# Performance work log

Hardware: AMD Instinct MI355X
Metric: run time of the kernel (lower is better)

Reference implementation:

```python
import jax, jax.numpy as jnp
import numpy as np


def setup_inputs() -> dict:
    key = jax.random.key(0)
    k1, k2 = jax.random.split(key)
    decoder_hidden = jax.random.normal(k1, (16, 1024, 1024), dtype=jnp.float32)
    encoder_outputs = jax.random.normal(k2, (16, 2048, 1024), dtype=jnp.float32)
    return {"decoder_hidden": decoder_hidden, "encoder_outputs": encoder_outputs}


def reference(decoder_hidden, encoder_outputs):
    # scores: [B, Q, K] = decoder_hidden @ encoder_outputs^T (no scaling, per source)
    scores = jnp.einsum('bqd,bkd->bqk', decoder_hidden, encoder_outputs)
    attn = jax.nn.softmax(scores, axis=-1)
    # context: [B, Q, D]
    context = jnp.einsum('bqk,bkd->bqd', attn, encoder_outputs)
    return (context, attn)
```

## Files before the change

### kernel.cpp

```cpp
#include <hip/hip_runtime.h>


typedef __attribute__((ext_vector_type(8))) short s8v;
typedef __attribute__((ext_vector_type(4))) float f32x4;
typedef __attribute__((ext_vector_type(8))) unsigned short us8;
typedef __attribute__((ext_vector_type(4))) unsigned short us4;

__device__ inline unsigned short f2bf(float f) {
    unsigned u = __builtin_bit_cast(unsigned, f);
    u += 0x7FFFu + ((u >> 16) & 1u);
    return (unsigned short)(u >> 16);
}
__device__ inline float bf2f(unsigned short h) {
    return __builtin_bit_cast(float, (unsigned)h << 16);
}

__device__ __forceinline__ s8v lds_read128(unsigned addr) {
    s8v d;
    asm volatile("ds_read_b128 %0, %1" : "=v"(d) : "v"(addr));
    return d;
}

__global__ __launch_bounds__(256)
void split_convert(const float* __restrict__ x, unsigned short* __restrict__ hi,
                   unsigned short* __restrict__ lo, int n4)
{
    int i = blockIdx.x * 256 + threadIdx.x;
    const int stride = gridDim.x * 256;
    for (; i < n4; i += stride) {
        const float4 v = reinterpret_cast<const float4*>(x)[i];
        us4 h, l;
        h.x = f2bf(v.x); l.x = f2bf(v.x - bf2f(h.x));
        h.y = f2bf(v.y); l.y = f2bf(v.y - bf2f(h.y));
        h.z = f2bf(v.z); l.z = f2bf(v.z - bf2f(h.z));
        h.w = f2bf(v.w); l.w = f2bf(v.w - bf2f(h.w));
        reinterpret_cast<us4*>(hi)[i] = h;
        reinterpret_cast<us4*>(lo)[i] = l;
    }
}

__global__ __launch_bounds__(256)
void split_convert_enc(const float* __restrict__ enc,
                       unsigned short* __restrict__ encH,
                       unsigned short* __restrict__ encL,
                       unsigned short* __restrict__ encT)
{
    __shared__ unsigned short S[64][72];
    const int b  = blockIdx.z;
    const int kt = blockIdx.x;
    const int dt = blockIdx.y;
    const int tid = threadIdx.x;

    const int r   = tid >> 2;
    const int c16 = (tid & 3) * 16;

    const size_t inoff = (size_t)b * 2048 * 1024 + (size_t)(kt * 64 + r) * 1024 + dt * 64 + c16;
    const float4* src = reinterpret_cast<const float4*>(enc + inoff);

    us8 h0, h1, l0, l1;
    #pragma unroll
    for (int q = 0; q < 2; ++q) {
        const float4 a = src[q * 2 + 0];
        const float4 c = src[q * 2 + 1];
        us8& h = q ? h1 : h0;
        us8& l = q ? l1 : l0;
        h[0] = f2bf(a.x); l[0] = f2bf(a.x - bf2f(h[0]));
        h[1] = f2bf(a.y); l[1] = f2bf(a.y - bf2f(h[1]));
        h[2] = f2bf(a.z); l[2] = f2bf(a.z - bf2f(h[2]));
        h[3] = f2bf(a.w); l[3] = f2bf(a.w - bf2f(h[3]));
        h[4] = f2bf(c.x); l[4] = f2bf(c.x - bf2f(h[4]));
        h[5] = f2bf(c.y); l[5] = f2bf(c.y - bf2f(h[5]));
        h[6] = f2bf(c.z); l[6] = f2bf(c.z - bf2f(h[6]));
        h[7] = f2bf(c.w); l[7] = f2bf(c.w - bf2f(h[7]));
    }
    *reinterpret_cast<us8*>(&encH[inoff])     = h0;
    *reinterpret_cast<us8*>(&encH[inoff + 8]) = h1;
    *reinterpret_cast<us8*>(&encL[inoff])     = l0;
    *reinterpret_cast<us8*>(&encL[inoff + 8]) = l1;
    *reinterpret_cast<us8*>(&S[r][c16])     = h0;
    *reinterpret_cast<us8*>(&S[r][c16 + 8]) = h1;
    __syncthreads();

    const int d   = tid >> 2;
    const int k16 = (tid & 3) * 16;
    us8 w0, w1;
    #pragma unroll
    for (int j = 0; j < 8; ++j) { w0[j] = S[k16 + j][d]; w1[j] = S[k16 + 8 + j][d]; }
    const size_t outoff = (size_t)b * 1024 * 2048 + (size_t)(dt * 64 + d) * 2048 + kt * 64 + k16;
    *reinterpret_cast<us8*>(&encT[outoff])     = w0;
    *reinterpret_cast<us8*>(&encT[outoff + 8]) = w1;
}

template<int NPASS, int KPP, int NXT, int NYT>
__global__ __launch_bounds__(512, 2)
void gemm_nt_256(const unsigned short* __restrict__ A0,
                 const unsigned short* __restrict__ A1,
                 const unsigned short* __restrict__ A2,
                 const unsigned short* __restrict__ B0,
                 const unsigned short* __restrict__ B1,
                 const unsigned short* __restrict__ B2,
                 float* __restrict__ Out,
                 const int ldA, const int ldB, const int ldO,
                 const long long sA, const long long sB, const long long sO)
{
    constexpr int TPP = KPP / 32;
    constexpr int NT  = NPASS * TPP;
    extern __shared__ unsigned short smem[];

    int flat = blockIdx.x + NXT * (blockIdx.y + NYT * (int)blockIdx.z);
    const int nwg = NXT * NYT * (int)gridDim.z;
    flat = (flat & 7) * (nwg >> 3) + (flat >> 3);
    const int nt = flat % NXT;
    const int mt = (flat / NXT) % NYT;
    const int b  = flat / (NXT * NYT);

    const int tid = threadIdx.x, lane = tid & 63, wid = tid >> 6;
    const int wm = wid >> 2, wn = wid & 3;

    const size_t arow = (size_t)b * sA + (size_t)(mt * 256) * ldA;
    const size_t brow = (size_t)b * sB + (size_t)(nt * 256) * ldB;
    const unsigned short* Ap0 = A0 + arow;
    const unsigned short* Ap1 = A1 + arow;
    const unsigned short* Ap2 = A2 + arow;
    const unsigned short* Bp0 = B0 + brow;
    const unsigned short* Bp1 = B1 + brow;
    const unsigned short* Bp2 = B2 + brow;

    const int ci0 = tid, ci1 = 512 + tid;
    const int r0 = ci0 >> 2, r1 = ci1 >> 2;
    const int cs0 = ((ci0 & 3) ^ ((r0 >> 1) & 3)) * 8;
    const int cs1 = ((ci1 & 3) ^ ((r1 >> 1) & 3)) * 8;
    const int aoff0 = r0 * ldA + cs0, aoff1 = r1 * ldA + cs1;
    const int boff0 = r0 * ldB + cs0, boff1 = r1 * ldB + cs1;
    const int wd0 = wid * 512;
    const int wd1 = 4096 + wid * 512;

    auto stageA = [&](int t) {
        const int p  = t / TPP;
        const int k0 = (t % TPP) * 32;
        const unsigned short* As = (p == 0) ? Ap0 : (p == 1 ? Ap1 : Ap2);
        unsigned short* d = smem + (t & 3) * 16384;
        __builtin_amdgcn_global_load_lds(
            (const __attribute__((address_space(1))) void*)(As + k0 + aoff0),
            (__attribute__((address_space(3))) void*)(d + wd0), 16, 0, 0);
        __builtin_amdgcn_global_load_lds(
            (const __attribute__((address_space(1))) void*)(As + k0 + aoff1),
            (__attribute__((address_space(3))) void*)(d + wd1), 16, 0, 0);
    };
    auto stageB = [&](int t) {
        const int p  = t / TPP;
        const int k0 = (t % TPP) * 32;
        const unsigned short* Bs = (p == 0) ? Bp0 : (p == 1 ? Bp1 : Bp2);
        unsigned short* d = smem + (t & 3) * 16384 + 8192;
        __builtin_amdgcn_global_load_lds(
            (const __attribute__((address_space(1))) void*)(Bs + k0 + boff0),
            (__attribute__((address_space(3))) void*)(d + wd0), 16, 0, 0);
        __builtin_amdgcn_global_load_lds(
            (const __attribute__((address_space(1))) void*)(Bs + k0 + boff1),
            (__attribute__((address_space(3))) void*)(d + wd1), 16, 0, 0);
    };

    const int fr = lane & 15;
    const int kc = lane >> 4;
    unsigned offA[8], offB[4];
    #pragma unroll
    for (int m = 0; m < 8; ++m) {
        const int R = wm * 128 + m * 16 + fr;
        offA[m] = (unsigned)(R * 64) + ((unsigned)(kc ^ ((R >> 1) & 3)) << 4);
    }
    #pragma unroll
    for (int n = 0; n < 4; ++n) {
        const int R = wn * 64 + n * 16 + fr;
        offB[n] = 16384u + (unsigned)(R * 64) + ((unsigned)(kc ^ ((R >> 1) & 3)) << 4);
    }

    const unsigned lds0 =
        (unsigned)(uintptr_t)(__attribute__((address_space(3))) unsigned short*)smem;

    f32x4 acc[8][4];
    #pragma unroll
    for (int m = 0; m < 8; ++m)
        #pragma unroll
        for (int n = 0; n < 4; ++n) acc[m][n] = (f32x4){0.f, 0.f, 0.f, 0.f};

    stageA(0); stageB(0); stageA(1); stageB(1); stageA(2); stageB(2);
    asm volatile("s_waitcnt vmcnt(4)" ::: "memory");
    __builtin_amdgcn_s_barrier();

    s8v fA[8], fB[4], gA[8], gB[4];
    #pragma unroll
    for (int n = 0; n < 4; ++n) fB[n] = lds_read128(lds0 + offB[n]);
    #pragma unroll
    for (int m = 0; m < 8; ++m) fA[m] = lds_read128(lds0 + offA[m]);

    auto issue_reads = [&](const int t, s8v (&na)[8], s8v (&nb)[4]) {
        const unsigned nbase = lds0 + (unsigned)((t + 1) & 3) * 32768u;
        #pragma unroll
        for (int n = 0; n < 4; ++n) nb[n] = lds_read128(nbase + offB[n]);
        #pragma unroll
        for (int m = 0; m < 8; ++m) na[m] = lds_read128(nbase + offA[m]);
    };
    auto do_mfma = [&](s8v (&ca)[8], s8v (&cb)[4]) {
        __builtin_amdgcn_s_setprio(1);
        #pragma unroll
        for (int m = 0; m < 8; ++m)
            #pragma unroll
            for (int n = 0; n < 4; ++n)
                acc[m][n] = __builtin_amdgcn_mfma_f32_16x16x32_bf16(ca[m], cb[n], acc[m][n], 0, 0, 0);
        __builtin_amdgcn_s_setprio(0);
    };
    auto tail_sync = [&](const int t) {
        if (t + 3 < NT)      asm volatile("s_waitcnt vmcnt(4)" ::: "memory");
        else if (t + 2 < NT) asm volatile("s_waitcnt vmcnt(0)" ::: "memory");
        __builtin_amdgcn_s_barrier();
    };

    auto bodyA = [&](const int t, s8v (&ca)[8], s8v (&cb)[4],
                     s8v (&na)[8], s8v (&nb)[4], const bool reads) {
        if (t + 3 < NT) { stageA(t + 3); stageB(t + 3); }
        if (reads) {
            issue_reads(t, na, nb);
            asm volatile("s_waitcnt lgkmcnt(12)" ::: "memory");
        } else {
            asm volatile("s_waitcnt lgkmcnt(0)" ::: "memory");
        }
        __builtin_amdgcn_sched_barrier(0);
        do_mfma(ca, cb);
        __builtin_amdgcn_sched_barrier(0);
        tail_sync(t);
    };
    auto bodyB = [&](const int t, s8v (&ca)[8], s8v (&cb)[4],
                     s8v (&na)[8], s8v (&nb)[4], const bool reads) {
        if (t + 3 < NT) { stageA(t + 3); stageB(t + 3); }
        asm volatile("s_waitcnt lgkmcnt(0)" ::: "memory");
        __builtin_amdgcn_sched_barrier(0);
        do_mfma(ca, cb);
        __builtin_amdgcn_sched_barrier(0);
        if (reads) issue_reads(t, na, nb);
        tail_sync(t);
    };

    if (wid < 4) {
        for (int tt = 0; tt < NT; tt += 2) {
            bodyA(tt,     fA, fB, gA, gB, true);
            bodyA(tt + 1, gA, gB, fA, fB, tt + 2 < NT);
        }
    } else {
        for (int tt = 0; tt < NT; tt += 2) {
            bodyB(tt,     fA, fB, gA, gB, true);
            bodyB(tt + 1, gA, gB, fA, fB, tt + 2 < NT);
        }
    }

    float* Ob = Out + (size_t)b * sO + (size_t)(mt * 256 + wm * 128) * ldO + nt * 256 + wn * 64;
    const int cr = (lane >> 4) << 2;
    const int cc = lane & 15;
    #pragma unroll
    for (int m = 0; m < 8; ++m)
        #pragma unroll
        for (int n = 0; n < 4; ++n)
            #pragma unroll
            for (int r = 0; r < 4; ++r)
                Ob[(size_t)(m * 16 + cr + r) * ldO + n * 16 + cc] = acc[m][n][r];
}

__global__ __launch_bounds__(256)
void softmax_rows_bf(float* __restrict__ P, unsigned short* __restrict__ Pb)
{
    float* p = P + (size_t)blockIdx.x * 2048;
    unsigned short* pb = Pb + (size_t)blockIdx.x * 2048;
    const int tid = threadIdx.x;

    float4 v0 = *reinterpret_cast<const float4*>(&p[tid * 4]);
    float4 v1 = *reinterpret_cast<const float4*>(&p[1024 + tid * 4]);

    float m = fmaxf(fmaxf(fmaxf(v0.x, v0.y), fmaxf(v0.z, v0.w)),
                    fmaxf(fmaxf(v1.x, v1.y), fmaxf(v1.z, v1.w)));
    #pragma unroll
    for (int off = 32; off; off >>= 1) m = fmaxf(m, __shfl_xor(m, off));

    __shared__ float red[8];
    const int wid = tid >> 6;
    if ((tid & 63) == 0) red[wid] = m;
    __syncthreads();
    m = fmaxf(fmaxf(red[0], red[1]), fmaxf(red[2], red[3]));

    v0.x = __expf(v0.x - m); v0.y = __expf(v0.y - m);
    v0.z = __expf(v0.z - m); v0.w = __expf(v0.w - m);
    v1.x = __expf(v1.x - m); v1.y = __expf(v1.y - m);
    v1.z = __expf(v1.z - m); v1.w = __expf(v1.w - m);

    float s = ((v0.x + v0.y) + (v0.z + v0.w)) + ((v1.x + v1.y) + (v1.z + v1.w));
    #pragma unroll
    for (int off = 32; off; off >>= 1) s += __shfl_xor(s, off);
    if ((tid & 63) == 0) red[4 + wid] = s;
    __syncthreads();
    const float inv = 1.0f / ((red[4] + red[5]) + (red[6] + red[7]));

    v0.x *= inv; v0.y *= inv; v0.z *= inv; v0.w *= inv;
    v1.x *= inv; v1.y *= inv; v1.z *= inv; v1.w *= inv;
    *reinterpret_cast<float4*>(&p[tid * 4]) = v0;
    *reinterpret_cast<float4*>(&p[1024 + tid * 4]) = v1;

    us4 h0, h1;
    h0.x = f2bf(v0.x); h0.y = f2bf(v0.y); h0.z = f2bf(v0.z); h0.w = f2bf(v0.w);
    h1.x = f2bf(v1.x); h1.y = f2bf(v1.y); h1.z = f2bf(v1.z); h1.w = f2bf(v1.w);
    *reinterpret_cast<us4*>(&pb[tid * 4]) = h0;
    *reinterpret_cast<us4*>(&pb[1024 + tid * 4]) = h1;
}

#define BM 128
#define BN 128
#define BK 32
#define LDT 132

template <bool TRANSB>
__global__ __launch_bounds__(256, 2)
void gemm_tile(const float* __restrict__ X, const float* __restrict__ Y,
               float* __restrict__ Out,
               int ldX, int ldY, int ldO, int KD,
               long long strideX, long long strideY, long long strideO)
{
    __shared__ float As[BK][LDT];
    __shared__ float Bs[BK][LDT];
    const int b  = blockIdx.z;
    const int mt = blockIdx.y;
    const int nt = blockIdx.x;
    const float* Xb = X + (size_t)b * strideX + (size_t)mt * BM * ldX;
    const float* Yb = TRANSB ? (Y + (size_t)b * strideY + (size_t)nt * BN * ldY)
                             : (Y + (size_t)b * strideY + (size_t)nt * BN);
    float* Ob = Out + (size_t)b * strideO + (size_t)mt * BM * ldO + (size_t)nt * BN;
    const int tid = threadIdx.x;
    const int tx = tid & 15;
    const int ty = tid >> 4;
    const int sr = tid >> 3;
    const int sc = (tid & 7) << 2;
    const int br = tid >> 5;
    const int bc = (tid & 31) << 2;
    float acc[8][8];
    #pragma unroll
    for (int i = 0; i < 8; ++i)
        #pragma unroll
        for (int j = 0; j < 8; ++j) acc[i][j] = 0.f;
    for (int k0 = 0; k0 < KD; k0 += BK) {
        #pragma unroll
        for (int p = 0; p < 4; ++p) {
            const float4 v = *reinterpret_cast<const float4*>(
                &Xb[(size_t)(sr + 32 * p) * ldX + k0 + sc]);
            As[sc + 0][sr + 32 * p] = v.x;
            As[sc + 1][sr + 32 * p] = v.y;
            As[sc + 2][sr + 32 * p] = v.z;
            As[sc + 3][sr + 32 * p] = v.w;
        }
        if (TRANSB) {
            #pragma unroll
            for (int p = 0; p < 4; ++p) {
                const float4 v = *reinterpret_cast<const float4*>(
                    &Yb[(size_t)(sr + 32 * p) * ldY + k0 + sc]);
                Bs[sc + 0][sr + 32 * p] = v.x;
                Bs[sc + 1][sr + 32 * p] = v.y;
                Bs[sc + 2][sr + 32 * p] = v.z;
                Bs[sc + 3][sr + 32 * p] = v.w;
            }
        } else {
            #pragma unroll
            for (int p = 0; p < 4; ++p) {
                const float4 v = *reinterpret_cast<const float4*>(
                    &Yb[(size_t)(k0 + br + 8 * p) * ldY + bc]);
                *reinterpret_cast<float4*>(&Bs[br + 8 * p][bc]) = v;
            }
        }
        __syncthreads();
        #pragma unroll 8
        for (int kk = 0; kk < BK; ++kk) {
            const float4 a0 = *reinterpret_cast<const float4*>(&As[kk][ty * 4]);
            const float4 a1 = *reinterpret_cast<const float4*>(&As[kk][64 + ty * 4]);
            const float4 b0 = *reinterpret_cast<const float4*>(&Bs[kk][tx * 4]);
            const float4 b1 = *reinterpret_cast<const float4*>(&Bs[kk][64 + tx * 4]);
            const float av[8] = {a0.x, a0.y, a0.z, a0.w, a1.x, a1.y, a1.z, a1.w};
            const float bv[8] = {b0.x, b0.y, b0.z, b0.w, b1.x, b1.y, b1.z, b1.w};
            #pragma unroll
            for (int i = 0; i < 8; ++i)
                #pragma unroll
                for (int j = 0; j < 8; ++j)
                    acc[i][j] = fmaf(av[i], bv[j], acc[i][j]);
        }
        __syncthreads();
    }
    #pragma unroll
    for (int i = 0; i < 8; ++i) {
        const int r = (i < 4) ? (ty * 4 + i) : (64 + ty * 4 + (i - 4));
        const float4 w0 = make_float4(acc[i][0], acc[i][1], acc[i][2], acc[i][3]);
        const float4 w1 = make_float4(acc[i][4], acc[i][5], acc[i][6], acc[i][7]);
        *reinterpret_cast<float4*>(&Ob[(size_t)r * ldO + tx * 4])      = w0;
        *reinterpret_cast<float4*>(&Ob[(size_t)r * ldO + 64 + tx * 4]) = w1;
    }
}

__global__ __launch_bounds__(256)
void softmax_rows(float* __restrict__ P)
{
    float* p = P + (size_t)blockIdx.x * 2048;
    const int tid = threadIdx.x;
    float4 v0 = *reinterpret_cast<const float4*>(&p[tid * 4]);
    float4 v1 = *reinterpret_cast<const float4*>(&p[1024 + tid * 4]);
    float m = fmaxf(fmaxf(fmaxf(v0.x, v0.y), fmaxf(v0.z, v0.w)),
                    fmaxf(fmaxf(v1.x, v1.y), fmaxf(v1.z, v1.w)));
    #pragma unroll
    for (int off = 32; off; off >>= 1) m = fmaxf(m, __shfl_xor(m, off));
    __shared__ float red[8];
    const int wid = tid >> 6;
    if ((tid & 63) == 0) red[wid] = m;
    __syncthreads();
    m = fmaxf(fmaxf(red[0], red[1]), fmaxf(red[2], red[3]));
    v0.x = __expf(v0.x - m); v0.y = __expf(v0.y - m);
    v0.z = __expf(v0.z - m); v0.w = __expf(v0.w - m);
    v1.x = __expf(v1.x - m); v1.y = __expf(v1.y - m);
    v1.z = __expf(v1.z - m); v1.w = __expf(v1.w - m);
    float s = ((v0.x + v0.y) + (v0.z + v0.w)) + ((v1.x + v1.y) + (v1.z + v1.w));
    #pragma unroll
    for (int off = 32; off; off >>= 1) s += __shfl_xor(s, off);
    if ((tid & 63) == 0) red[4 + wid] = s;
    __syncthreads();
    const float inv = 1.0f / ((red[4] + red[5]) + (red[6] + red[7]));
    v0.x *= inv; v0.y *= inv; v0.z *= inv; v0.w *= inv;
    v1.x *= inv; v1.y *= inv; v1.z *= inv; v1.w *= inv;
    *reinterpret_cast<float4*>(&p[tid * 4]) = v0;
    *reinterpret_cast<float4*>(&p[1024 + tid * 4]) = v1;
}

extern "C" void kernel_launch(void* const* d_in, const int* in_sizes, int n_in,
                              void* d_out, int out_size, void* d_ws, size_t ws_size,
                              hipStream_t stream)
{
    const float* dec = (const float*)d_in[0];
    const float* enc = (const float*)d_in[1];
    float* ctx  = (float*)d_out;
    float* attn = ctx + (size_t)16 * 1024 * 1024;

    const long long DECN = 16LL * 1024 * 1024;
    const long long ENCN = 16LL * 2048 * 1024;
    const size_t NEED = (size_t)(2 * DECN + 4 * ENCN) * 2;

    if (ws_size >= NEED) {
        unsigned short* decH  = (unsigned short*)d_ws;
        unsigned short* decL  = decH + DECN;
        unsigned short* encH  = decL + DECN;
        unsigned short* encL  = encH + ENCN;
        unsigned short* encT  = encL + ENCN;
        unsigned short* attnB = encT + ENCN;

        hipFuncSetAttribute((const void*)&gemm_nt_256<3, 1024, 8, 4>,
                            hipFuncAttributeMaxDynamicSharedMemorySize, 131072);
        hipFuncSetAttribute((const void*)&gemm_nt_256<1, 2048, 4, 4>,
                            hipFuncAttributeMaxDynamicSharedMemorySize, 131072);

        split_convert<<<2048, 256, 0, stream>>>(dec, decH, decL, (int)(DECN / 4));
        split_convert_enc<<<dim3(32, 16, 16), 256, 0, stream>>>(enc, encH, encL, encT);

        gemm_nt_256<3, 1024, 8, 4><<<dim3(8, 4, 16), 512, 131072, stream>>>(
            decH, decH, decL, encH, encL, encH, attn,
            1024, 1024, 2048,
            1024LL * 1024, 2048LL * 1024, 1024LL * 2048);

        softmax_rows_bf<<<16 * 1024, 256, 0, stream>>>(attn, attnB);

        gemm_nt_256<1, 2048, 4, 4><<<dim3(4, 4, 16), 512, 131072, stream>>>(
            attnB, attnB, attnB, encT, encT, encT, ctx,
            2048, 2048, 1024,
            1024LL * 2048, 1024LL * 2048, 1024LL * 1024);
    } else {
        gemm_tile<true><<<dim3(2048 / BN, 1024 / BM, 16), 256, 0, stream>>>(
            dec, enc, attn, 1024, 1024, 2048, 1024,
            1024LL * 1024, 2048LL * 1024, 1024LL * 2048);
        softmax_rows<<<dim3(16 * 1024), 256, 0, stream>>>(attn);
        gemm_tile<false><<<dim3(1024 / BN, 1024 / BM, 16), 256, 0, stream>>>(
            attn, enc, ctx, 2048, 1024, 1024, 2048,
            1024LL * 2048, 2048LL * 1024, 1024LL * 1024);
    }
}
```

Before: 419.7 us.

## Restructure bf16 GEMM mainloop into 8-phase ping-pong schedule with 64-wide K tiles

Replaces the 4-stage, 32-wide-K GEMM pipeline (split into producer/consumer wave roles) with a double-buffered 64-wide-K tile. Each iteration is broken into eight phases in which all waves interleave quarter-tile LDS reads, global-to-LDS loads and MFMA bursts, with barriers between phases. The LDS swizzle changes to an 8-way XOR over 128-byte rows. The aim is to hide LDS and global latency behind MFMA work and cut barrier overhead per K step. The cost is many more barriers per iteration and only two buffers instead of four, so global loads have less time to arrive.

```diff
diff --git a/kernel.cpp b/kernel.cpp
--- a/kernel.cpp
+++ b/kernel.cpp
@@ -19,6 +19,52 @@
     s8v d;
     asm volatile("ds_read_b128 %0, %1" : "=v"(d) : "v"(addr));
     return d;
+}
+__device__ __forceinline__ void gld16(const unsigned short* src, unsigned short* dstLds) {
+    __builtin_amdgcn_global_load_lds(
+        (const __attribute__((address_space(1))) void*)src,
+        (__attribute__((address_space(3))) void*)dstLds, 16, 0, 0);
+}
+
+#define LGKM(n)  asm volatile("s_waitcnt lgkmcnt(" #n ")" ::: "memory")
+#define VMC(n)   asm volatile("s_waitcnt vmcnt(" #n ")" ::: "memory")
+#define SB0      __builtin_amdgcn_sched_barrier(0)
+#define BARR     __builtin_amdgcn_s_barrier()
+
+template<int MH, int NH>
+__device__ __forceinline__ void mfma16(f32x4 (&acc)[8][4], const s8v (&a)[8], const s8v (&b)[4])
+{
+    __builtin_amdgcn_s_setprio(1);
+    #pragma unroll
+    for (int kf = 0; kf < 2; ++kf)
+        #pragma unroll
+        for (int mp = 0; mp < 4; ++mp)
+            #pragma unroll
+            for (int np = 0; np < 2; ++np)
+                acc[MH * 4 + mp][NH * 2 + np] = __builtin_amdgcn_mfma_f32_16x16x32_bf16(
+                    a[mp * 2 + kf], b[np * 2 + kf], acc[MH * 4 + mp][NH * 2 + np], 0, 0, 0);
+    __builtin_amdgcn_s_setprio(0);
+}
+
+template<int D, int MH>
+__device__ __forceinline__ void readA(s8v (&a)[8], unsigned abase, unsigned cb0, unsigned cb1)
+{
+    const unsigned base = abase + D * 65536u + MH * 8192u;
+    #pragma unroll
+    for (int mp = 0; mp < 4; ++mp) {
+        a[mp * 2 + 0] = lds_read128(base + mp * 2048u + cb0);
+        a[mp * 2 + 1] = lds_read128(base + mp * 2048u + cb1);
+    }
+}
+template<int D, int NH>
+__device__ __forceinline__ void readB(s8v (&b)[4], unsigned bbase, unsigned cb0, unsigned cb1)
+{
+    const unsigned base = bbase + D * 65536u + NH * 4096u;
+    #pragma unroll
+    for (int np = 0; np < 2; ++np) {
+        b[np * 2 + 0] = lds_read128(base + np * 2048u + cb0);
+        b[np * 2 + 1] = lds_read128(base + np * 2048u + cb1);
+    }
 }
 
 __global__ __launch_bounds__(256)
@@ -91,20 +137,20 @@
     *reinterpret_cast<us8*>(&encT[outoff + 8]) = w1;
 }
 
-template<int NPASS, int KPP, int NXT, int NYT>
+template<int NPASS, int KSP, int NXT, int NYT>
 __global__ __launch_bounds__(512, 2)
-void gemm_nt_256(const unsigned short* __restrict__ A0,
-                 const unsigned short* __restrict__ A1,
-                 const unsigned short* __restrict__ A2,
-                 const unsigned short* __restrict__ B0,
-                 const unsigned short* __restrict__ B1,
-                 const unsigned short* __restrict__ B2,
+void gemm_nt_8ph(const unsigned short* __restrict__ A0p,
+                 const unsigned short* __restrict__ A1p,
+                 const unsigned short* __restrict__ A2p,
+                 const unsigned short* __restrict__ B0p,
+                 const unsigned short* __restrict__ B1p,
+                 const unsigned short* __restrict__ B2p,
                  float* __restrict__ Out,
                  const int ldA, const int ldB, const int ldO,
                  const long long sA, const long long sB, const long long sO)
 {
-    constexpr int TPP = KPP / 32;
-    constexpr int NT  = NPASS * TPP;
+    constexpr int NK    = NPASS * KSP;
+    constexpr int NITER = NK / 2;
     extern __shared__ unsigned short smem[];
 
     int flat = blockIdx.x + NXT * (blockIdx.y + NYT * (int)blockIdx.z);
@@ -116,66 +162,45 @@
 
     const int tid = threadIdx.x, lane = tid & 63, wid = tid >> 6;
     const int wm = wid >> 2, wn = wid & 3;
+    const int fr = lane & 15, kc = lane >> 4;
 
     const size_t arow = (size_t)b * sA + (size_t)(mt * 256) * ldA;
     const size_t brow = (size_t)b * sB + (size_t)(nt * 256) * ldB;
-    const unsigned short* Ap0 = A0 + arow;
-    const unsigned short* Ap1 = A1 + arow;
-    const unsigned short* Ap2 = A2 + arow;
-    const unsigned short* Bp0 = B0 + brow;
-    const unsigned short* Bp1 = B1 + brow;
-    const unsigned short* Bp2 = B2 + brow;
-
-    const int ci0 = tid, ci1 = 512 + tid;
-    const int r0 = ci0 >> 2, r1 = ci1 >> 2;
-    const int cs0 = ((ci0 & 3) ^ ((r0 >> 1) & 3)) * 8;
-    const int cs1 = ((ci1 & 3) ^ ((r1 >> 1) & 3)) * 8;
-    const int aoff0 = r0 * ldA + cs0, aoff1 = r1 * ldA + cs1;
-    const int boff0 = r0 * ldB + cs0, boff1 = r1 * ldB + cs1;
-    const int wd0 = wid * 512;
-    const int wd1 = 4096 + wid * 512;
-
-    auto stageA = [&](int t) {
-        const int p  = t / TPP;
-        const int k0 = (t % TPP) * 32;
-        const unsigned short* As = (p == 0) ? Ap0 : (p == 1 ? Ap1 : Ap2);
-        unsigned short* d = smem + (t & 3) * 16384;
-        __builtin_amdgcn_global_load_lds(
-            (const __attribute__((address_space(1))) void*)(As + k0 + aoff0),
-            (__attribute__((address_space(3))) void*)(d + wd0), 16, 0, 0);
-        __builtin_amdgcn_global_load_lds(
-            (const __attribute__((address_space(1))) void*)(As + k0 + aoff1),
-            (__attribute__((address_space(3))) void*)(d + wd1), 16, 0, 0);
+    const unsigned short* Ap0 = A0p + arow;
+    const unsigned short* Ap1 = A1p + arow;
+    const unsigned short* Ap2 = A2p + arow;
+    const unsigned short* Bp0 = B0p + brow;
+    const unsigned short* Bp1 = B1p + brow;
+    const unsigned short* Bp2 = B2p + brow;
+
+    const int srow = tid >> 3;
+    const int sc   = ((tid & 7) ^ (srow & 7)) * 8;
+    const int offA0 = srow * ldA + sc, offA1 = offA0 + 64 * ldA;
+    const int offB0 = srow * ldB + sc, offB1 = offB0 + 64 * ldB;
+
+    auto STAGEA = [&](int ks, int h) {
+        const int p = ks / KSP;
+        const unsigned short* s = ((p == 0) ? Ap0 : (p == 1) ? Ap1 : Ap2)
+                                  + (size_t)(h * 128) * ldA + (ks - p * KSP) * 64;
+        unsigned short* d = smem + ((ks & 1) * 32768 + h * 8192) + wid * 512;
+        gld16(s + offA0, d);
+        gld16(s + offA1, d + 4096);
     };
-    auto stageB = [&](int t) {
-        const int p  = t / TPP;
-        const int k0 = (t % TPP) * 32;
-        const unsigned short* Bs = (p == 0) ? Bp0 : (p == 1 ? Bp1 : Bp2);
-        unsigned short* d = smem + (t & 3) * 16384 + 8192;
-        __builtin_amdgcn_global_load_lds(
-            (const __attribute__((address_space(1))) void*)(Bs + k0 + boff0),
-            (__attribute__((address_space(3))) void*)(d + wd0), 16, 0, 0);
-        __builtin_amdgcn_global_load_lds(
-            (const __attribute__((address_space(1))) void*)(Bs + k0 + boff1),
-            (__attribute__((address_space(3))) void*)(d + wd1), 16, 0, 0);
+    auto STAGEB = [&](int ks, int h) {
+        const int p = ks / KSP;
+        const unsigned short* s = ((p == 0) ? Bp0 : (p == 1) ? Bp1 : Bp2)
+                                  + (size_t)(h * 128) * ldB + (ks - p * KSP) * 64;
+        unsigned short* d = smem + ((ks & 1) * 32768 + 16384 + h * 8192) + wid * 512;
+        gld16(s + offB0, d);
+        gld16(s + offB1, d + 4096);
     };
-
-    const int fr = lane & 15;
-    const int kc = lane >> 4;
-    unsigned offA[8], offB[4];
-    #pragma unroll
-    for (int m = 0; m < 8; ++m) {
-        const int R = wm * 128 + m * 16 + fr;
-        offA[m] = (unsigned)(R * 64) + ((unsigned)(kc ^ ((R >> 1) & 3)) << 4);
-    }
-    #pragma unroll
-    for (int n = 0; n < 4; ++n) {
-        const int R = wn * 64 + n * 16 + fr;
-        offB[n] = 16384u + (unsigned)(R * 64) + ((unsigned)(kc ^ ((R >> 1) & 3)) << 4);
-    }
 
     const unsigned lds0 =
         (unsigned)(uintptr_t)(__attribute__((address_space(3))) unsigned short*)smem;
+    const unsigned cb0 = (unsigned)((kc ^ (fr & 7)) * 16);
+    const unsigned cb1 = cb0 ^ 64u;
+    const unsigned abase = lds0 + wm * 16384u + fr * 128u;
+    const unsigned bbase = lds0 + 32768u + (wn >> 1) * 16384u + (wn & 1) * 8192u + fr * 128u;
 
     f32x4 acc[8][4];
     #pragma unroll
@@ -183,74 +208,61 @@
         #pragma unroll
         for (int n = 0; n < 4; ++n) acc[m][n] = (f32x4){0.f, 0.f, 0.f, 0.f};
 
-    stageA(0); stageB(0); stageA(1); stageB(1); stageA(2); stageB(2);
-    asm volatile("s_waitcnt vmcnt(4)" ::: "memory");
-    __builtin_amdgcn_s_barrier();
-
-    s8v fA[8], fB[4], gA[8], gB[4];
-    #pragma unroll
-    for (int n = 0; n < 4; ++n) fB[n] = lds_read128(lds0 + offB[n]);
-    #pragma unroll
-    for (int m = 0; m < 8; ++m) fA[m] = lds_read128(lds0 + offA[m]);
-
-    auto issue_reads = [&](const int t, s8v (&na)[8], s8v (&nb)[4]) {
-        const unsigned nbase = lds0 + (unsigned)((t + 1) & 3) * 32768u;
-        #pragma unroll
-        for (int n = 0; n < 4; ++n) nb[n] = lds_read128(nbase + offB[n]);
-        #pragma unroll
-        for (int m = 0; m < 8; ++m) na[m] = lds_read128(nbase + offA[m]);
+    s8v a[8], b0[4], b1[4];
+
+    STAGEA(0, 0); STAGEA(0, 1); STAGEB(0, 0); STAGEB(0, 1);
+    STAGEB(1, 0); STAGEB(1, 1); STAGEA(1, 0);
+    VMC(6);
+    BARR;
+
+    auto iter = [&](const int t, const bool last) {
+        const int ks0 = 2 * t;
+        readA<0, 0>(a, abase, cb0, cb1);
+        readB<0, 0>(b0, bbase, cb0, cb1);
+        STAGEA(ks0 + 1, 1);
+        LGKM(8); SB0; BARR; LGKM(0); SB0;
+        mfma16<0, 0>(acc, a, b0);
+        BARR;
+        readB<0, 1>(b1, bbase, cb0, cb1);
+        if (!last) STAGEB(ks0 + 2, 0);
+        SB0; BARR; LGKM(0); SB0;
+        mfma16<0, 1>(acc, a, b1);
+        BARR;
+        readA<0, 1>(a, abase, cb0, cb1);
+        if (!last) STAGEB(ks0 + 2, 1);
+        LGKM(4); SB0; BARR; LGKM(0); SB0;
+        mfma16<1, 0>(acc, a, b0);
+        BARR;
+        if (!last) STAGEA(ks0 + 2, 0);
+        if (last) { VMC(0); } else { VMC(6); }
+        SB0; BARR;
+        mfma16<1, 1>(acc, a, b1);
+        BARR;
+        readA<1, 0>(a, abase, cb0, cb1);
+        readB<1, 0>(b0, bbase, cb0, cb1);
+        if (!last) STAGEA(ks0 + 2, 1);
+        LGKM(8); SB0; BARR; LGKM(0); SB0;
+        mfma16<0, 0>(acc, a, b0);
+        BARR;
+        readB<1, 1>(b1, bbase, cb0, cb1);
+        if (!last) STAGEB(ks0 + 3, 0);
+        SB0; BARR; LGKM(0); SB0;
+        mfma16<0, 1>(acc, a, b1);
+        BARR;
+        readA<1, 1>(a, abase, cb0, cb1);
+        if (!last) STAGEB(ks0 + 3, 1);
+        LGKM(4); SB0; BARR; LGKM(0); SB0;
+        mfma16<1, 0>(acc, a, b0);
+        BARR;
+        if (!last) STAGEA(ks0 + 3, 0);
+        if (last) { VMC(0); } else { VMC(6); }
+        SB0; BARR;
+        mfma16<1, 1>(acc, a, b1);
+        BARR;
     };
-    auto do_mfma = [&](s8v (&ca)[8], s8v (&cb)[4]) {
-        __builtin_amdgcn_s_setprio(1);
-        #pragma unroll
-        for (int m = 0; m < 8; ++m)
-            #pragma unroll
-            for (int n = 0; n < 4; ++n)
-                acc[m][n] = __builtin_amdgcn_mfma_f32_16x16x32_bf16(ca[m], cb[n], acc[m][n], 0, 0, 0);
-        __builtin_amdgcn_s_setprio(0);
-    };
-    auto tail_sync = [&](const int t) {
-        if (t + 3 < NT)      asm volatile("s_waitcnt vmcnt(4)" ::: "memory");
-        else if (t + 2 < NT) asm volatile("s_waitcnt vmcnt(0)" ::: "memory");
-        __builtin_amdgcn_s_barrier();
-    };
-
-    auto bodyA = [&](const int t, s8v (&ca)[8], s8v (&cb)[4],
-                     s8v (&na)[8], s8v (&nb)[4], const bool reads) {
-        if (t + 3 < NT) { stageA(t + 3); stageB(t + 3); }
-        if (reads) {
-            issue_reads(t, na, nb);
-            asm volatile("s_waitcnt lgkmcnt(12)" ::: "memory");
-        } else {
-            asm volatile("s_waitcnt lgkmcnt(0)" ::: "memory");
-        }
-        __builtin_amdgcn_sched_barrier(0);
-        do_mfma(ca, cb);
-        __builtin_amdgcn_sched_barrier(0);
-        tail_sync(t);
-    };
-    auto bodyB = [&](const int t, s8v (&ca)[8], s8v (&cb)[4],
-                     s8v (&na)[8], s8v (&nb)[4], const bool reads) {
-        if (t + 3 < NT) { stageA(t + 3); stageB(t + 3); }
-        asm volatile("s_waitcnt lgkmcnt(0)" ::: "memory");
-        __builtin_amdgcn_sched_barrier(0);
-        do_mfma(ca, cb);
-        __builtin_amdgcn_sched_barrier(0);
-        if (reads) issue_reads(t, na, nb);
-        tail_sync(t);
-    };
-
-    if (wid < 4) {
-        for (int tt = 0; tt < NT; tt += 2) {
-            bodyA(tt,     fA, fB, gA, gB, true);
-            bodyA(tt + 1, gA, gB, fA, fB, tt + 2 < NT);
-        }
-    } else {
-        for (int tt = 0; tt < NT; tt += 2) {
-            bodyB(tt,     fA, fB, gA, gB, true);
-            bodyB(tt + 1, gA, gB, fA, fB, tt + 2 < NT);
-        }
-    }
+
+    for (int t = 0; t < NITER - 1; ++t) iter(t, false);
+    iter(NITER - 1, true);
 
     float* Ob = Out + (size_t)b * sO + (size_t)(mt * 256 + wm * 128) * ldO + nt * 256 + wn * 64;
     const int cr = (lane >> 4) << 2;
@@ -450,22 +462,22 @@
         unsigned short* encT  = encL + ENCN;
         unsigned short* attnB = encT + ENCN;
 
-        hipFuncSetAttribute((const void*)&gemm_nt_256<3, 1024, 8, 4>,
+        hipFuncSetAttribute((const void*)&gemm_nt_8ph<3, 16, 8, 4>,
                             hipFuncAttributeMaxDynamicSharedMemorySize, 131072);
-        hipFuncSetAttribute((const void*)&gemm_nt_256<1, 2048, 4, 4>,
+        hipFuncSetAttribute((const void*)&gemm_nt_8ph<1, 32, 4, 4>,
                             hipFuncAttributeMaxDynamicSharedMemorySize, 131072);
 
         split_convert<<<2048, 256, 0, stream>>>(dec, decH, decL, (int)(DECN / 4));
         split_convert_enc<<<dim3(32, 16, 16), 256, 0, stream>>>(enc, encH, encL, encT);
 
-        gemm_nt_256<3, 1024, 8, 4><<<dim3(8, 4, 16), 512, 131072, stream>>>(
+        gemm_nt_8ph<3, 16, 8, 4><<<dim3(8, 4, 16), 512, 131072, stream>>>(
             decH, decH, decL, encH, encL, encH, attn,
             1024, 1024, 2048,
             1024LL * 1024, 2048LL * 1024, 1024LL * 2048);
 
         softmax_rows_bf<<<16 * 1024, 256, 0, stream>>>(attn, attnB);
 
-        gemm_nt_256<1, 2048, 4, 4><<<dim3(4, 4, 16), 512, 131072, stream>>>(
+        gemm_nt_8ph<1, 32, 4, 4><<<dim3(4, 4, 16), 512, 131072, stream>>>(
             attnB, attnB, attnB, encT, encT, encT, ctx,
             2048, 2048, 1024,
             1024LL * 2048, 1024LL * 2048, 1024LL * 1024);
```

Measured after the change: 471.8 us. 12.4% more time.

## Fuse three split-bf16 passes of first GEMM into one K loop reusing tiles

Applied to the files above, without the earlier changes.

Replaces the three-pass gemm_nt_256 for the scores GEMM (hi*hi, hi*lo, lo*hi, each streaming K separately) with a single K loop. Each iteration stages Ah, Al, Bh and Bl tiles together in a double-buffered LDS layout and issues all three MFMA products from them. This cuts global/LDS reloads of the shared hi operands and loop overhead across the passes. In exchange it goes from a 4-stage to a 2-stage buffer, adds extra barriers per tile, waits for each prefetch with vmcnt(0), and holds more fragment registers.

```diff
diff --git a/kernel.cpp b/kernel.cpp
--- a/kernel.cpp
+++ b/kernel.cpp
@@ -20,6 +20,16 @@
     asm volatile("ds_read_b128 %0, %1" : "=v"(d) : "v"(addr));
     return d;
 }
+__device__ __forceinline__ void gld16(const unsigned short* src, unsigned short* dstLds) {
+    __builtin_amdgcn_global_load_lds(
+        (const __attribute__((address_space(1))) void*)src,
+        (__attribute__((address_space(3))) void*)dstLds, 16, 0, 0);
+}
+
+#define LGKM0    asm volatile("s_waitcnt lgkmcnt(0)" ::: "memory")
+#define VMC(n)   asm volatile("s_waitcnt vmcnt(" #n ")" ::: "memory")
+#define SB0      __builtin_amdgcn_sched_barrier(0)
+#define BARR     __builtin_amdgcn_s_barrier()
 
 __global__ __launch_bounds__(256)
 void split_convert(const float* __restrict__ x, unsigned short* __restrict__ hi,
@@ -91,6 +101,134 @@
     *reinterpret_cast<us8*>(&encT[outoff + 8]) = w1;
 }
 
+template<int KTILES, int NXT, int NYT>
+__global__ __launch_bounds__(512, 2)
+void gemm1_quad(const unsigned short* __restrict__ Ah_, const unsigned short* __restrict__ Al_,
+                const unsigned short* __restrict__ Bh_, const unsigned short* __restrict__ Bl_,
+                float* __restrict__ Out,
+                const int ldA, const int ldB, const int ldO,
+                const long long sA, const long long sB, const long long sO)
+{
+    extern __shared__ unsigned short smem[];
+
+    int flat = blockIdx.x + NXT * (blockIdx.y + NYT * (int)blockIdx.z);
+    const int nwg = NXT * NYT * (int)gridDim.z;
+    flat = (flat & 7) * (nwg >> 3) + (flat >> 3);
+    const int nt = flat % NXT;
+    const int mt = (flat / NXT) % NYT;
+    const int b  = flat / (NXT * NYT);
+
+    const int tid = threadIdx.x, lane = tid & 63, wid = tid >> 6;
+    const int wm = wid >> 2, wn = wid & 3;
+
+    const size_t arow = (size_t)b * sA + (size_t)(mt * 256) * ldA;
+    const size_t brow = (size_t)b * sB + (size_t)(nt * 256) * ldB;
+    const unsigned short* Ahb = Ah_ + arow;
+    const unsigned short* Alb = Al_ + arow;
+    const unsigned short* Bhb = Bh_ + brow;
+    const unsigned short* Blb = Bl_ + brow;
+
+    const int ci0 = tid, ci1 = 512 + tid;
+    const int r0 = ci0 >> 2, r1 = ci1 >> 2;
+    const int cs0 = ((ci0 & 3) ^ ((r0 >> 1) & 3)) * 8;
+    const int cs1 = ((ci1 & 3) ^ ((r1 >> 1) & 3)) * 8;
+    const int aoff0 = r0 * ldA + cs0, aoff1 = r1 * ldA + cs1;
+    const int boff0 = r0 * ldB + cs0, boff1 = r1 * ldB + cs1;
+    const int wd0 = wid * 512, wd1 = 4096 + wid * 512;
+
+    auto stage_set = [&](int t) {
+        const int k0 = t * 32;
+        unsigned short* s = smem + (t & 1) * 32768;
+        gld16(Ahb + k0 + aoff0, s + wd0);          gld16(Ahb + k0 + aoff1, s + wd1);
+        gld16(Alb + k0 + aoff0, s + 8192 + wd0);   gld16(Alb + k0 + aoff1, s + 8192 + wd1);
+        gld16(Bhb + k0 + boff0, s + 16384 + wd0);  gld16(Bhb + k0 + boff1, s + 16384 + wd1);
+        gld16(Blb + k0 + boff0, s + 24576 + wd0);  gld16(Blb + k0 + boff1, s + 24576 + wd1);
+    };
+
+    const int fr = lane & 15, kc = lane >> 4;
+    unsigned offA[8], offB[4];
+    #pragma unroll
+    for (int m = 0; m < 8; ++m) {
+        const int R = wm * 128 + m * 16 + fr;
+        offA[m] = (unsigned)(R * 64) + ((unsigned)(kc ^ ((R >> 1) & 3)) << 4);
+    }
+    #pragma unroll
+    for (int n = 0; n < 4; ++n) {
+        const int R = wn * 64 + n * 16 + fr;
+        offB[n] = (unsigned)(R * 64) + ((unsigned)(kc ^ ((R >> 1) & 3)) << 4);
+    }
+
+    const unsigned lds0 =
+        (unsigned)(uintptr_t)(__attribute__((address_space(3))) unsigned short*)smem;
+
+    f32x4 acc[8][4];
+    #pragma unroll
+    for (int m = 0; m < 8; ++m)
+        #pragma unroll
+        for (int n = 0; n < 4; ++n) acc[m][n] = (f32x4){0.f, 0.f, 0.f, 0.f};
+
+    s8v ah[8], al[8], bh[4], bl[4];
+
+    stage_set(0);
+    VMC(0); BARR;
+
+    for (int t = 0; t < KTILES; ++t) {
+        const unsigned base = lds0 + (unsigned)(t & 1) * 65536u;
+        const bool notlast = (t + 1 < KTILES);
+
+        #pragma unroll
+        for (int n = 0; n < 4; ++n) bh[n] = lds_read128(base + 32768u + offB[n]);
+        #pragma unroll
+        for (int m = 0; m < 8; ++m) ah[m] = lds_read128(base + offA[m]);
+        if (notlast) stage_set(t + 1);
+        BARR; LGKM0; SB0;
+        __builtin_amdgcn_s_setprio(1);
+        #pragma unroll
+        for (int m = 0; m < 8; ++m)
+            #pragma unroll
+            for (int n = 0; n < 4; ++n)
+                acc[m][n] = __builtin_amdgcn_mfma_f32_16x16x32_bf16(ah[m], bh[n], acc[m][n], 0, 0, 0);
+        __builtin_amdgcn_s_setprio(0);
+        BARR;
+
+        #pragma unroll
+        for (int n = 0; n < 4; ++n) bl[n] = lds_read128(base + 49152u + offB[n]);
+        BARR; LGKM0; SB0;
+        __builtin_amdgcn_s_setprio(1);
+        #pragma unroll
+        for (int m = 0; m < 8; ++m)
+            #pragma unroll
+            for (int n = 0; n < 4; ++n)
+                acc[m][n] = __builtin_amdgcn_mfma_f32_16x16x32_bf16(ah[m], bl[n], acc[m][n], 0, 0, 0);
+        __builtin_amdgcn_s_setprio(0);
+        BARR;
+
+        #pragma unroll
+        for (int m = 0; m < 8; ++m) al[m] = lds_read128(base + 16384u + offA[m]);
+        BARR; LGKM0; SB0;
+        __builtin_amdgcn_s_setprio(1);
+        #pragma unroll
+        for (int m = 0; m < 8; ++m)
+            #pragma unroll
+            for (int n = 0; n < 4; ++n)
+                acc[m][n] = __builtin_amdgcn_mfma_f32_16x16x32_bf16(al[m], bh[n], acc[m][n], 0, 0, 0);
+        __builtin_amdgcn_s_setprio(0);
+        if (notlast) VMC(0);
+        BARR;
+    }
+
+    float* Ob = Out + (size_t)b * sO + (size_t)(mt * 256 + wm * 128) * ldO + nt * 256 + wn * 64;
+    const int cr = (lane >> 4) << 2;
+    const int cc = lane & 15;
+    #pragma unroll
+    for (int m = 0; m < 8; ++m)
+        #pragma unroll
+        for (int n = 0; n < 4; ++n)
+            #pragma unroll
+            for (int r = 0; r < 4; ++r)
+                Ob[(size_t)(m * 16 + cr + r) * ldO + n * 16 + cc] = acc[m][n][r];
+}
+
 template<int NPASS, int KPP, int NXT, int NYT>
 __global__ __launch_bounds__(512, 2)
 void gemm_nt_256(const unsigned short* __restrict__ A0,
@@ -140,24 +278,16 @@
         const int k0 = (t % TPP) * 32;
         const unsigned short* As = (p == 0) ? Ap0 : (p == 1 ? Ap1 : Ap2);
         unsigned short* d = smem + (t & 3) * 16384;
-        __builtin_amdgcn_global_load_lds(
-            (const __attribute__((address_space(1))) void*)(As + k0 + aoff0),
-            (__attribute__((address_space(3))) void*)(d + wd0), 16, 0, 0);
-        __builtin_amdgcn_global_load_lds(
-            (const __attribute__((address_space(1))) void*)(As + k0 + aoff1),
-            (__attribute__((address_space(3))) void*)(d + wd1), 16, 0, 0);
+        gld16(As + k0 + aoff0, d + wd0);
+        gld16(As + k0 + aoff1, d + wd1);
     };
     auto stageB = [&](int t) {
         const int p  = t / TPP;
         const int k0 = (t % TPP) * 32;
         const unsigned short* Bs = (p == 0) ? Bp0 : (p == 1 ? Bp1 : Bp2);
         unsigned short* d = smem + (t & 3) * 16384 + 8192;
-        __builtin_amdgcn_global_load_lds(
-            (const __attribute__((address_space(1))) void*)(Bs + k0 + boff0),
-            (__attribute__((address_space(3))) void*)(d + wd0), 16, 0, 0);
-        __builtin_amdgcn_global_load_lds(
-            (const __attribute__((address_space(1))) void*)(Bs + k0 + boff1),
-            (__attribute__((address_space(3))) void*)(d + wd1), 16, 0, 0);
+        gld16(Bs + k0 + boff0, d + wd0);
+        gld16(Bs + k0 + boff1, d + wd1);
     };
 
     const int fr = lane & 15;
@@ -450,7 +580,7 @@
         unsigned short* encT  = encL + ENCN;
         unsigned short* attnB = encT + ENCN;
 
-        hipFuncSetAttribute((const void*)&gemm_nt_256<3, 1024, 8, 4>,
+        hipFuncSetAttribute((const void*)&gemm1_quad<32, 8, 4>,
                             hipFuncAttributeMaxDynamicSharedMemorySize, 131072);
         hipFuncSetAttribute((const void*)&gemm_nt_256<1, 2048, 4, 4>,
                             hipFuncAttributeMaxDynamicSharedMemorySize, 131072);
@@ -458,8 +588,8 @@
         split_convert<<<2048, 256, 0, stream>>>(dec, decH, decL, (int)(DECN / 4));
         split_convert_enc<<<dim3(32, 16, 16), 256, 0, stream>>>(enc, encH, encL, encT);
 
-        gemm_nt_256<3, 1024, 8, 4><<<dim3(8, 4, 16), 512, 131072, stream>>>(
-            decH, decH, decL, encH, encL, encH, attn,
+        gemm1_quad<32, 8, 4><<<dim3(8, 4, 16), 512, 131072, stream>>>(
+            decH, decL, encH, encL, attn,
             1024, 1024, 2048,
             1024LL * 1024, 2048LL * 1024, 1024LL * 2048);
 
```

Result: no change. 411.6 us, median of 2 (-1.9%).
